# Kernel optimization log

Measured on AMD Instinct MI355X. Metric: run time of the kernel, lower is better.

Reference implementation:

```python
import jax, jax.numpy as jnp
import numpy as np

B, D, E, H, O, TOPK = 16384, 256, 8, 128, 1, 2
THRESHOLD = 0.5
NUM_SCALES = 3
TAUS = np.linspace(5.0, 20.0, NUM_SCALES)  # MSLIFNeuron tau_range=(5,20), num_scales=3


def setup_inputs() -> dict:
    key = jax.random.key(0)
    ks = jax.random.split(key, 10)
    s = lambda fan: 1.0 / np.sqrt(fan)
    return {
        "features": jax.random.normal(ks[0], (B, D), jnp.float32),
        "Wg": jax.random.normal(ks[1], (D, E), jnp.float32) * s(D),
        "W1": jax.random.normal(ks[2], (E, D, H), jnp.float32) * s(D),
        "b1": jnp.zeros((E, H), jnp.float32),
        "Wp": jax.random.normal(ks[3], (E, H, H), jnp.float32) * s(H),
        "bp": jnp.zeros((E, H), jnp.float32),
        "mix_logit": jnp.zeros((E,), jnp.float32),
        "Wo": jax.random.normal(ks[4], (E, H, O), jnp.float32) * s(H),
        "bo": jnp.zeros((E, O), jnp.float32),
    }


def _mslif_spikes(x):
    # multi-scale LIF, single step from zero state: v_s = x * (1 - exp(-dt/tau_s))
    decays = jnp.asarray(1.0 - np.exp(-1.0 / TAUS), x.dtype)  # [S]
    v = x[:, None, :] * decays[None, :, None]                  # [B,S,D]
    return (v > THRESHOLD).astype(x.dtype).mean(axis=1)        # [B,D]


def reference(features, Wg, W1, b1, Wp, bp, mix_logit, Wo, bo):
    # gating: softmax over experts, top-k renormalized
    gate = jax.nn.softmax(features @ Wg, axis=-1)              # [B,E]
    _, idx = jax.lax.top_k(gate, TOPK)                         # [B,K]
    mask = jax.nn.one_hot(idx, E, dtype=gate.dtype).sum(1)     # [B,E]
    w = gate * mask
    w = w / (w.sum(-1, keepdims=True) + 1e-10)

    # spike generator (computed in expert forward; not used downstream)
    _spikes = _mslif_spikes(features)

    # NeuroDynArch expert: static core + plasticity mix
    core = jax.nn.relu(jnp.einsum('bd,edh->beh', features, W1) + b1[None])
    plast = jnp.tanh(jnp.einsum('beh,ehk->bek', core, Wp) + bp[None])
    mix = jax.nn.sigmoid(mix_logit)[None, :, None]             # [1,E,1]
    mixed = core * (1.0 - mix) + plast * mix                   # [B,E,H]
    out_e = jnp.einsum('beh,eho->beo', mixed, Wo) + bo[None]   # [B,E,O]
    return jnp.einsum('beo,be->bo', out_e, w)                  # [B,O]
```

## Files before the change

kernel.cpp:

```cpp
#include <hip/hip_runtime.h>

#define BB 16384
#define DD 256
#define EE 8
#define HH 128

typedef __attribute__((ext_vector_type(8))) short short8;
typedef __attribute__((ext_vector_type(4))) float f32x4;

__device__ __forceinline__ ushort f2bf(float f){
    const unsigned u = __float_as_uint(f);
    return (ushort)((u + 0x7fffu + ((u >> 16) & 1u)) >> 16);
}
__device__ __forceinline__ float bf2f(ushort s){
    return __uint_as_float(((unsigned)s) << 16);
}
__device__ __forceinline__ float fast_tanh(float v){
    v = fminf(fmaxf(v, -15.0f), 15.0f);
    const float a = __expf(2.0f * v);
    return (a - 1.0f) / (a + 1.0f);
}
__device__ __forceinline__ void gload_lds16(const void* g, void* l){
    __builtin_amdgcn_global_load_lds(
        (const __attribute__((address_space(1))) unsigned*)g,
        (__attribute__((address_space(3))) unsigned*)l, 16, 0, 0);
}

__global__ __launch_bounds__(256) void transpose_kernel(
    const float* __restrict__ W1, const float* __restrict__ Wp,
    ushort* __restrict__ W1t, ushort* __restrict__ Wpt, int* __restrict__ counts)
{
    __shared__ float tile[64 * 68];
    int b = blockIdx.x;
    const int t = threadIdx.x;
    if (b == 0 && t < EE) counts[t] = 0;
    const float* src; ushort* dst; int K;
    int k0, h0;
    if (b < 64){
        const int e = b >> 3, kt = (b >> 1) & 3, ht = b & 1;
        src = W1 + (size_t)e * DD * HH;  dst = W1t + (size_t)e * HH * DD;
        K = DD; k0 = kt * 64; h0 = ht * 64;
    } else {
        b -= 64;
        const int e = b >> 2, kt = (b >> 1) & 1, ht = b & 1;
        src = Wp + (size_t)e * HH * HH;  dst = Wpt + (size_t)e * HH * HH;
        K = HH; k0 = kt * 64; h0 = ht * 64;
    }
    #pragma unroll
    for (int j = 0; j < 4; j++){
        const int idx = t + 256 * j;
        const int kk = idx >> 4, hh = (idx & 15) * 4;
        const float4 v = *(const float4*)(src + (size_t)(k0 + kk) * HH + h0 + hh);
        *(float4*)&tile[kk * 68 + hh] = v;
    }
    __syncthreads();
    #pragma unroll
    for (int j = 0; j < 4; j++){
        const int idx = t + 256 * j;
        const int hh = idx >> 4, kk = (idx & 15) * 4;
        ushort4 o;
        o.x = f2bf(tile[(kk + 0) * 68 + hh]);
        o.y = f2bf(tile[(kk + 1) * 68 + hh]);
        o.z = f2bf(tile[(kk + 2) * 68 + hh]);
        o.w = f2bf(tile[(kk + 3) * 68 + hh]);
        *(ushort4*)&dst[(size_t)(h0 + hh) * K + k0 + kk] = o;
    }
}

__global__ __launch_bounds__(256) void routing_kernel(
    const float* __restrict__ x, const float* __restrict__ Wg,
    int* __restrict__ counts, int* __restrict__ rowids, float* __restrict__ wgts,
    float* __restrict__ out, ushort* __restrict__ xbf)
{
    __shared__ __align__(16) float WgT[EE][DD];
    __shared__ int   le[64];
    __shared__ float lw[64];
    __shared__ int   loff[64];
    __shared__ int   lcount[EE];
    __shared__ int   lbase[EE];

    const int t = threadIdx.x;
    const int rowBase = blockIdx.x * 32;
    if (t < 32) out[rowBase + t] = 0.0f;
    {
        const float4* g = (const float4*)(Wg + t * EE);
        const float4 a = g[0], b = g[1];
        WgT[0][t] = a.x; WgT[1][t] = a.y; WgT[2][t] = a.z; WgT[3][t] = a.w;
        WgT[4][t] = b.x; WgT[5][t] = b.y; WgT[6][t] = b.z; WgT[7][t] = b.w;
    }
    if (t < EE) lcount[t] = 0;
    __syncthreads();

    const int lane = t & 63;
    const int wid  = t >> 6;

    for (int it = 0; it < 8; it++){
        const int slot = wid * 8 + it;
        const int row  = rowBase + slot;
        const float4 xv = *(const float4*)(x + row * DD + lane * 4);
        {
            ushort4 o;
            o.x = f2bf(xv.x); o.y = f2bf(xv.y); o.z = f2bf(xv.z); o.w = f2bf(xv.w);
            *(ushort4*)&xbf[(size_t)row * DD + lane * 4] = o;
        }
        float p[EE];
        #pragma unroll
        for (int e = 0; e < EE; e++){
            const float4 w = *(const float4*)&WgT[e][lane * 4];
            p[e] = xv.x * w.x + xv.y * w.y + xv.z * w.z + xv.w * w.w;
        }
        #pragma unroll
        for (int off = 32; off >= 1; off >>= 1){
            #pragma unroll
            for (int e = 0; e < EE; e++) p[e] += __shfl_down(p[e], off, 64);
        }
        if (lane == 0){
            int e0 = 0; float l0 = p[0];
            #pragma unroll
            for (int e = 1; e < EE; e++){ if (p[e] > l0){ l0 = p[e]; e0 = e; } }
            int e1 = -1; float l1 = -3.0e38f;
            #pragma unroll
            for (int e = 0; e < EE; e++){ if (e != e0 && p[e] > l1){ l1 = p[e]; e1 = e; } }
            const float tt  = __expf(l1 - l0);
            const float inv = 1.0f / (1.0f + tt);
            le[slot]      = e0;  lw[slot]      = inv;
            le[32 + slot] = e1;  lw[32 + slot] = tt * inv;
        }
    }
    __syncthreads();
    if (t < 64) loff[t] = atomicAdd(&lcount[le[t]], 1);
    __syncthreads();
    if (t < EE) lbase[t] = atomicAdd(&counts[t], lcount[t]);
    __syncthreads();
    if (t < 64){
        const int e   = le[t];
        const int pos = lbase[e] + loff[t];
        rowids[e * BB + pos] = rowBase + (t & 31);
        wgts[e * BB + pos]   = lw[t];
    }
}

#define CS_S 136

__global__ __launch_bounds__(256, 2) void expert_kernel(
    const ushort* __restrict__ xbf,
    const ushort* __restrict__ W1t, const float* __restrict__ b1,
    const ushort* __restrict__ Wpt, const float* __restrict__ bp,
    const float* __restrict__ mix_logit,
    const float* __restrict__ Wo, const float* __restrict__ bo,
    const int* __restrict__ counts, const int* __restrict__ rowids,
    const float* __restrict__ wgts, float* __restrict__ out)
{
    const int me    = blockIdx.y;
    const int cnt   = counts[me];
    const int start = blockIdx.x * 64;
    if (start >= cnt) return;

    __shared__ ushort Xs[64 * DD];
    __shared__ ushort coreS[64 * CS_S];
    __shared__ int   rid_s[64];
    __shared__ float w_s[64];

    const int t = threadIdx.x;
    if (t < 64){
        const int idx = start + t;
        if (idx < cnt){ rid_s[t] = rowids[me * BB + idx]; w_s[t] = wgts[me * BB + idx]; }
        else          { rid_s[t] = 0;                     w_s[t] = 0.0f; }
    }
    __syncthreads();

    const int lane = t & 63;
    const int w    = t >> 6;

    {
        const int rsub = lane >> 5;
        const int c    = lane & 31;
        #pragma unroll
        for (int i = 0; i < 8; i++){
            const int row = w * 16 + i * 2 + rsub;
            const int sc  = c ^ (row & 7);
            const ushort* gp = xbf + (size_t)rid_s[row] * DD + sc * 8;
            gload_lds16(gp, &Xs[(w * 16 + i * 2) * DD]);
        }
    }
    asm volatile("s_waitcnt vmcnt(0)" ::: "memory");
    __syncthreads();

    const int m16  = lane & 15;
    const int q    = lane >> 4;
    const int r0   = 32 * (w >> 1);
    const int c0   = 64 * (w & 1);
    const int swz  = m16 & 7;

    f32x4 acc[2][4];
    #pragma unroll
    for (int ct = 0; ct < 4; ct++){
        const float bj = b1[me * HH + c0 + ct * 16 + m16];
        #pragma unroll
        for (int rt = 0; rt < 2; rt++) acc[rt][ct] = (f32x4){bj, bj, bj, bj};
    }
    const ushort* W1te = W1t + (size_t)me * HH * DD;
    #pragma unroll
    for (int ks = 0; ks < 8; ks++){
        const int kc = ks * 4 + q;
        short8 af[2], bf[4];
        #pragma unroll
        for (int rt = 0; rt < 2; rt++)
            af[rt] = *(const short8*)&Xs[(r0 + rt * 16 + m16) * DD + ((kc ^ swz) * 8)];
        #pragma unroll
        for (int ct = 0; ct < 4; ct++)
            bf[ct] = *(const short8*)&W1te[(size_t)(c0 + ct * 16 + m16) * DD + ks * 32 + q * 8];
        #pragma unroll
        for (int rt = 0; rt < 2; rt++)
            #pragma unroll
            for (int ct = 0; ct < 4; ct++)
                acc[rt][ct] = __builtin_amdgcn_mfma_f32_16x16x32_bf16(af[rt], bf[ct], acc[rt][ct], 0, 0, 0);
    }

    #pragma unroll
    for (int rt = 0; rt < 2; rt++)
        #pragma unroll
        for (int ct = 0; ct < 4; ct++)
            #pragma unroll
            for (int j = 0; j < 4; j++){
                const int row = r0 + rt * 16 + q * 4 + j;
                const int col = c0 + ct * 16 + m16;
                coreS[row * CS_S + col] = f2bf(fmaxf(acc[rt][ct][j], 0.0f));
            }
    __syncthreads();

    #pragma unroll
    for (int ct = 0; ct < 4; ct++){
        const float bj = bp[me * HH + c0 + ct * 16 + m16];
        #pragma unroll
        for (int rt = 0; rt < 2; rt++) acc[rt][ct] = (f32x4){bj, bj, bj, bj};
    }
    const ushort* Wpte = Wpt + (size_t)me * HH * HH;
    #pragma unroll
    for (int ks = 0; ks < 4; ks++){
        const int k0 = ks * 32;
        short8 af[2], bf[4];
        #pragma unroll
        for (int rt = 0; rt < 2; rt++)
            af[rt] = *(const short8*)&coreS[(r0 + rt * 16 + m16) * CS_S + k0 + q * 8];
        #pragma unroll
        for (int ct = 0; ct < 4; ct++)
            bf[ct] = *(const short8*)&Wpte[(size_t)(c0 + ct * 16 + m16) * HH + k0 + q * 8];
        #pragma unroll
        for (int rt = 0; rt < 2; rt++)
            #pragma unroll
            for (int ct = 0; ct < 4; ct++)
                acc[rt][ct] = __builtin_amdgcn_mfma_f32_16x16x32_bf16(af[rt], bf[ct], acc[rt][ct], 0, 0, 0);
    }

    const float mv  = 1.0f / (1.0f + __expf(-mix_logit[me]));
    const float om  = 1.0f - mv;
    const float bov = bo[me];
    float wo[4];
    #pragma unroll
    for (int ct = 0; ct < 4; ct++) wo[ct] = Wo[me * HH + c0 + ct * 16 + m16];

    float red[2][4];
    #pragma unroll
    for (int rt = 0; rt < 2; rt++)
        #pragma unroll
        for (int j = 0; j < 4; j++){
            float s = 0.0f;
            const int row = r0 + rt * 16 + q * 4 + j;
            #pragma unroll
            for (int ct = 0; ct < 4; ct++){
                const int col = c0 + ct * 16 + m16;
                const float pl = fast_tanh(acc[rt][ct][j]);
                const float cv = bf2f(coreS[row * CS_S + col]);
                s = fmaf(om * cv + mv * pl, wo[ct], s);
            }
            red[rt][j] = s;
        }
    #pragma unroll
    for (int off = 8; off >= 1; off >>= 1)
        #pragma unroll
        for (int rt = 0; rt < 2; rt++)
            #pragma unroll
            for (int j = 0; j < 4; j++)
                red[rt][j] += __shfl_xor(red[rt][j], off, 64);

    if (m16 == 0){
        const float bb = (c0 == 0) ? bov : 0.0f;
        #pragma unroll
        for (int rt = 0; rt < 2; rt++)
            #pragma unroll
            for (int j = 0; j < 4; j++){
                const int row = r0 + rt * 16 + q * 4 + j;
                const float ww = w_s[row];
                if (ww != 0.0f) atomicAdd(&out[rid_s[row]], (red[rt][j] + bb) * ww);
            }
    }
}

extern "C" void kernel_launch(void* const* d_in, const int* in_sizes, int n_in,
                              void* d_out, int out_size, void* d_ws, size_t ws_size,
                              hipStream_t stream) {
    (void)in_sizes; (void)n_in; (void)out_size; (void)ws_size;
    const float* x   = (const float*)d_in[0];
    const float* Wg  = (const float*)d_in[1];
    const float* W1  = (const float*)d_in[2];
    const float* b1  = (const float*)d_in[3];
    const float* Wp  = (const float*)d_in[4];
    const float* bp  = (const float*)d_in[5];
    const float* ml  = (const float*)d_in[6];
    const float* Wo  = (const float*)d_in[7];
    const float* bo  = (const float*)d_in[8];
    float* out = (float*)d_out;

    char* ws = (char*)d_ws;
    int*    counts = (int*)ws;
    int*    rowids = (int*)(ws + 256);
    float*  wgts   = (float*)(ws + 256 + (size_t)EE * BB * 4);
    ushort* W1t    = (ushort*)(ws + 256 + 2 * (size_t)EE * BB * 4);
    ushort* Wpt    = W1t + (size_t)EE * HH * DD;
    ushort* xbf    = Wpt + (size_t)EE * HH * HH;

    transpose_kernel<<<96, 256, 0, stream>>>(W1, Wp, W1t, Wpt, counts);
    routing_kernel<<<BB / 32, 256, 0, stream>>>(x, Wg, counts, rowids, wgts, out, xbf);
    expert_kernel<<<dim3(BB / 64, EE), 256, 0, stream>>>(
        xbf, W1t, b1, Wpt, bp, ml, Wo, bo, counts, rowids, wgts, out);
}
```

Measured before the change: 120.2 us.

## Fuse transpose, routing and expert kernels into one cooperative persistent launch

Merges the three kernels into a single cooperative-groups kernel of 512 persistent blocks. Grid-wide syncs replace the kernel boundaries, and the expert phase loops over (expert, chunk) work items. The per-expert counters are padded onto separate cache lines to reduce atomic contention. The aim is to cut launch overhead and inter-kernel gaps, at the cost of grid-sync latency and occupancy limits, with a fallback to the three-kernel path if a cooperative launch is not possible.

```diff
diff --git a/kernel.cpp b/kernel.cpp
--- a/kernel.cpp
+++ b/kernel.cpp
@@ -1,9 +1,15 @@
 #include <hip/hip_runtime.h>
+#include <hip/hip_cooperative_groups.h>
+
+namespace cg = cooperative_groups;
 
 #define BB 16384
 #define DD 256
 #define EE 8
 #define HH 128
+#define NBLK 512
+#define CPAD 32
+#define CS_S 136
 
 typedef __attribute__((ext_vector_type(8))) short short8;
 typedef __attribute__((ext_vector_type(4))) float f32x4;
@@ -26,14 +32,23 @@
         (__attribute__((address_space(3))) unsigned*)l, 16, 0, 0);
 }
 
-__global__ __launch_bounds__(256) void transpose_kernel(
+struct RT {
+    float WgT[EE][DD];
+    int   le[64];
+    float lw[64];
+    int   loff[64];
+    int   lcount[EE];
+    int   lbase[EE];
+};
+struct P1 { float tile[64 * 68]; RT rt; };
+struct P3 { ushort Xs[64 * DD]; ushort coreS[64 * CS_S];
+            int rid[64]; float wgt[64]; };
+union ShU { P1 p1; P3 p3; };
+
+__device__ __forceinline__ void transpose_body(int b, int t,
     const float* __restrict__ W1, const float* __restrict__ Wp,
-    ushort* __restrict__ W1t, ushort* __restrict__ Wpt, int* __restrict__ counts)
-{
-    __shared__ float tile[64 * 68];
-    int b = blockIdx.x;
-    const int t = threadIdx.x;
-    if (b == 0 && t < EE) counts[t] = 0;
+    ushort* __restrict__ W1t, ushort* __restrict__ Wpt, float* tile)
+{
     const float* src; ushort* dst; int K;
     int k0, h0;
     if (b < 64){
@@ -67,28 +82,19 @@
     }
 }
 
-__global__ __launch_bounds__(256) void routing_kernel(
+__device__ __forceinline__ void routing_p1(int bid, int t,
     const float* __restrict__ x, const float* __restrict__ Wg,
-    int* __restrict__ counts, int* __restrict__ rowids, float* __restrict__ wgts,
-    float* __restrict__ out, ushort* __restrict__ xbf)
-{
-    __shared__ __align__(16) float WgT[EE][DD];
-    __shared__ int   le[64];
-    __shared__ float lw[64];
-    __shared__ int   loff[64];
-    __shared__ int   lcount[EE];
-    __shared__ int   lbase[EE];
-
-    const int t = threadIdx.x;
-    const int rowBase = blockIdx.x * 32;
+    float* __restrict__ out, ushort* __restrict__ xbf, RT* rt)
+{
+    const int rowBase = bid * 32;
     if (t < 32) out[rowBase + t] = 0.0f;
     {
         const float4* g = (const float4*)(Wg + t * EE);
         const float4 a = g[0], b = g[1];
-        WgT[0][t] = a.x; WgT[1][t] = a.y; WgT[2][t] = a.z; WgT[3][t] = a.w;
-        WgT[4][t] = b.x; WgT[5][t] = b.y; WgT[6][t] = b.z; WgT[7][t] = b.w;
-    }
-    if (t < EE) lcount[t] = 0;
+        rt->WgT[0][t] = a.x; rt->WgT[1][t] = a.y; rt->WgT[2][t] = a.z; rt->WgT[3][t] = a.w;
+        rt->WgT[4][t] = b.x; rt->WgT[5][t] = b.y; rt->WgT[6][t] = b.z; rt->WgT[7][t] = b.w;
+    }
+    if (t < EE) rt->lcount[t] = 0;
     __syncthreads();
 
     const int lane = t & 63;
@@ -106,7 +112,7 @@
         float p[EE];
         #pragma unroll
         for (int e = 0; e < EE; e++){
-            const float4 w = *(const float4*)&WgT[e][lane * 4];
+            const float4 w = *(const float4*)&rt->WgT[e][lane * 4];
             p[e] = xv.x * w.x + xv.y * w.y + xv.z * w.z + xv.w * w.w;
         }
         #pragma unroll
@@ -123,49 +129,42 @@
             for (int e = 0; e < EE; e++){ if (e != e0 && p[e] > l1){ l1 = p[e]; e1 = e; } }
             const float tt  = __expf(l1 - l0);
             const float inv = 1.0f / (1.0f + tt);
-            le[slot]      = e0;  lw[slot]      = inv;
-            le[32 + slot] = e1;  lw[32 + slot] = tt * inv;
-        }
-    }
-    __syncthreads();
-    if (t < 64) loff[t] = atomicAdd(&lcount[le[t]], 1);
-    __syncthreads();
-    if (t < EE) lbase[t] = atomicAdd(&counts[t], lcount[t]);
+            rt->le[slot]      = e0;  rt->lw[slot]      = inv;
+            rt->le[32 + slot] = e1;  rt->lw[32 + slot] = tt * inv;
+        }
+    }
+}
+
+__device__ __forceinline__ void routing_p2(int bid, int t,
+    int* counts, int* __restrict__ rowids, float* __restrict__ wgts, RT* rt)
+{
+    __syncthreads();
+    if (t < 64) rt->loff[t] = atomicAdd(&rt->lcount[rt->le[t]], 1);
+    __syncthreads();
+    if (t < EE) rt->lbase[t] = atomicAdd(&counts[t * CPAD], rt->lcount[t]);
     __syncthreads();
     if (t < 64){
-        const int e   = le[t];
-        const int pos = lbase[e] + loff[t];
-        rowids[e * BB + pos] = rowBase + (t & 31);
-        wgts[e * BB + pos]   = lw[t];
-    }
-}
-
-#define CS_S 136
-
-__global__ __launch_bounds__(256, 2) void expert_kernel(
+        const int e   = rt->le[t];
+        const int pos = rt->lbase[e] + rt->loff[t];
+        rowids[e * BB + pos] = bid * 32 + (t & 31);
+        wgts[e * BB + pos]   = rt->lw[t];
+    }
+}
+
+__device__ void expert_chunk(int me, int start, int cnt, int t,
     const ushort* __restrict__ xbf,
     const ushort* __restrict__ W1t, const float* __restrict__ b1,
     const ushort* __restrict__ Wpt, const float* __restrict__ bp,
     const float* __restrict__ mix_logit,
     const float* __restrict__ Wo, const float* __restrict__ bo,
-    const int* __restrict__ counts, const int* __restrict__ rowids,
-    const float* __restrict__ wgts, float* __restrict__ out)
-{
-    const int me    = blockIdx.y;
-    const int cnt   = counts[me];
-    const int start = blockIdx.x * 64;
-    if (start >= cnt) return;
-
-    __shared__ ushort Xs[64 * DD];
-    __shared__ ushort coreS[64 * CS_S];
-    __shared__ int   rid_s[64];
-    __shared__ float w_s[64];
-
-    const int t = threadIdx.x;
+    const int* __restrict__ rowids, const float* __restrict__ wgts,
+    float* __restrict__ out, P3* p3)
+{
+    __syncthreads();
     if (t < 64){
         const int idx = start + t;
-        if (idx < cnt){ rid_s[t] = rowids[me * BB + idx]; w_s[t] = wgts[me * BB + idx]; }
-        else          { rid_s[t] = 0;                     w_s[t] = 0.0f; }
+        if (idx < cnt){ p3->rid[t] = rowids[me * BB + idx]; p3->wgt[t] = wgts[me * BB + idx]; }
+        else          { p3->rid[t] = 0;                     p3->wgt[t] = 0.0f; }
     }
     __syncthreads();
 
@@ -179,8 +178,8 @@
         for (int i = 0; i < 8; i++){
             const int row = w * 16 + i * 2 + rsub;
             const int sc  = c ^ (row & 7);
-            const ushort* gp = xbf + (size_t)rid_s[row] * DD + sc * 8;
-            gload_lds16(gp, &Xs[(w * 16 + i * 2) * DD]);
+            const ushort* gp = xbf + (size_t)p3->rid[row] * DD + sc * 8;
+            gload_lds16(gp, &p3->Xs[(w * 16 + i * 2) * DD]);
         }
     }
     asm volatile("s_waitcnt vmcnt(0)" ::: "memory");
@@ -203,18 +202,18 @@
     #pragma unroll
     for (int ks = 0; ks < 8; ks++){
         const int kc = ks * 4 + q;
-        short8 af[2], bf[4];
-        #pragma unroll
-        for (int rt = 0; rt < 2; rt++)
-            af[rt] = *(const short8*)&Xs[(r0 + rt * 16 + m16) * DD + ((kc ^ swz) * 8)];
+        short8 af[2], bfr[4];
+        #pragma unroll
+        for (int rt = 0; rt < 2; rt++)
+            af[rt] = *(const short8*)&p3->Xs[(r0 + rt * 16 + m16) * DD + ((kc ^ swz) * 8)];
         #pragma unroll
         for (int ct = 0; ct < 4; ct++)
-            bf[ct] = *(const short8*)&W1te[(size_t)(c0 + ct * 16 + m16) * DD + ks * 32 + q * 8];
+            bfr[ct] = *(const short8*)&W1te[(size_t)(c0 + ct * 16 + m16) * DD + ks * 32 + q * 8];
         #pragma unroll
         for (int rt = 0; rt < 2; rt++)
             #pragma unroll
             for (int ct = 0; ct < 4; ct++)
-                acc[rt][ct] = __builtin_amdgcn_mfma_f32_16x16x32_bf16(af[rt], bf[ct], acc[rt][ct], 0, 0, 0);
+                acc[rt][ct] = __builtin_amdgcn_mfma_f32_16x16x32_bf16(af[rt], bfr[ct], acc[rt][ct], 0, 0, 0);
     }
 
     #pragma unroll
@@ -225,7 +224,7 @@
             for (int j = 0; j < 4; j++){
                 const int row = r0 + rt * 16 + q * 4 + j;
                 const int col = c0 + ct * 16 + m16;
-                coreS[row * CS_S + col] = f2bf(fmaxf(acc[rt][ct][j], 0.0f));
+                p3->coreS[row * CS_S + col] = f2bf(fmaxf(acc[rt][ct][j], 0.0f));
             }
     __syncthreads();
 
@@ -239,18 +238,18 @@
     #pragma unroll
     for (int ks = 0; ks < 4; ks++){
         const int k0 = ks * 32;
-        short8 af[2], bf[4];
-        #pragma unroll
-        for (int rt = 0; rt < 2; rt++)
-            af[rt] = *(const short8*)&coreS[(r0 + rt * 16 + m16) * CS_S + k0 + q * 8];
+        short8 af[2], bfr[4];
+        #pragma unroll
+        for (int rt = 0; rt < 2; rt++)
+            af[rt] = *(const short8*)&p3->coreS[(r0 + rt * 16 + m16) * CS_S + k0 + q * 8];
         #pragma unroll
         for (int ct = 0; ct < 4; ct++)
-            bf[ct] = *(const short8*)&Wpte[(size_t)(c0 + ct * 16 + m16) * HH + k0 + q * 8];
+            bfr[ct] = *(const short8*)&Wpte[(size_t)(c0 + ct * 16 + m16) * HH + k0 + q * 8];
         #pragma unroll
         for (int rt = 0; rt < 2; rt++)
             #pragma unroll
             for (int ct = 0; ct < 4; ct++)
-                acc[rt][ct] = __builtin_amdgcn_mfma_f32_16x16x32_bf16(af[rt], bf[ct], acc[rt][ct], 0, 0, 0);
+                acc[rt][ct] = __builtin_amdgcn_mfma_f32_16x16x32_bf16(af[rt], bfr[ct], acc[rt][ct], 0, 0, 0);
     }
 
     const float mv  = 1.0f / (1.0f + __expf(-mix_logit[me]));
@@ -271,7 +270,7 @@
             for (int ct = 0; ct < 4; ct++){
                 const int col = c0 + ct * 16 + m16;
                 const float pl = fast_tanh(acc[rt][ct][j]);
-                const float cv = bf2f(coreS[row * CS_S + col]);
+                const float cv = bf2f(p3->coreS[row * CS_S + col]);
                 s = fmaf(om * cv + mv * pl, wo[ct], s);
             }
             red[rt][j] = s;
@@ -291,10 +290,82 @@
             #pragma unroll
             for (int j = 0; j < 4; j++){
                 const int row = r0 + rt * 16 + q * 4 + j;
-                const float ww = w_s[row];
-                if (ww != 0.0f) atomicAdd(&out[rid_s[row]], (red[rt][j] + bb) * ww);
+                const float ww = p3->wgt[row];
+                if (ww != 0.0f) atomicAdd(&out[p3->rid[row]], (red[rt][j] + bb) * ww);
             }
     }
+}
+
+__global__ __launch_bounds__(256, 2) void fused_kernel(
+    const float* __restrict__ x, const float* __restrict__ Wg,
+    const float* __restrict__ W1, const float* __restrict__ b1,
+    const float* __restrict__ Wp, const float* __restrict__ bp,
+    const float* __restrict__ ml, const float* __restrict__ Wo,
+    const float* __restrict__ bo,
+    int* counts, int* rowids, float* wgts,
+    ushort* W1t, ushort* Wpt, ushort* xbf, float* out)
+{
+    __shared__ ShU sh;
+    const int bid = blockIdx.x;
+    const int t   = threadIdx.x;
+
+    if (bid == 0 && t < EE) counts[t * CPAD] = 0;
+    if (bid < 96) transpose_body(bid, t, W1, Wp, W1t, Wpt, sh.p1.tile);
+    routing_p1(bid, t, x, Wg, out, xbf, &sh.p1.rt);
+
+    cg::this_grid().sync();
+
+    routing_p2(bid, t, counts, rowids, wgts, &sh.p1.rt);
+
+    cg::this_grid().sync();
+
+    #pragma unroll 1
+    for (int v = bid; v < EE * 256; v += NBLK){
+        const int me    = v & 7;
+        const int start = (v >> 3) * 64;
+        const int cnt   = counts[me * CPAD];
+        if (start < cnt)
+            expert_chunk(me, start, cnt, t, xbf, W1t, b1, Wpt, bp, ml, Wo, bo,
+                         rowids, wgts, out, &sh.p3);
+    }
+}
+
+__global__ __launch_bounds__(256) void transpose_kernel(
+    const float* __restrict__ W1, const float* __restrict__ Wp,
+    ushort* __restrict__ W1t, ushort* __restrict__ Wpt, int* __restrict__ counts)
+{
+    __shared__ float tile[64 * 68];
+    const int t = threadIdx.x;
+    if (blockIdx.x == 0 && t < EE) counts[t * CPAD] = 0;
+    transpose_body(blockIdx.x, t, W1, Wp, W1t, Wpt, tile);
+}
+
+__global__ __launch_bounds__(256) void routing_kernel(
+    const float* __restrict__ x, const float* __restrict__ Wg,
+    int* counts, int* __restrict__ rowids, float* __restrict__ wgts,
+    float* __restrict__ out, ushort* __restrict__ xbf)
+{
+    __shared__ RT rt;
+    routing_p1(blockIdx.x, threadIdx.x, x, Wg, out, xbf, &rt);
+    routing_p2(blockIdx.x, threadIdx.x, counts, rowids, wgts, &rt);
+}
+
+__global__ __launch_bounds__(256, 2) void expert_kernel(
+    const ushort* __restrict__ xbf,
+    const ushort* __restrict__ W1t, const float* __restrict__ b1,
+    const ushort* __restrict__ Wpt, const float* __restrict__ bp,
+    const float* __restrict__ ml,
+    const float* __restrict__ Wo, const float* __restrict__ bo,
+    const int* __restrict__ counts, const int* __restrict__ rowids,
+    const float* __restrict__ wgts, float* __restrict__ out)
+{
+    const int me    = blockIdx.y;
+    const int cnt   = counts[me * CPAD];
+    const int start = blockIdx.x * 64;
+    if (start >= cnt) return;
+    __shared__ P3 p3;
+    expert_chunk(me, start, cnt, threadIdx.x, xbf, W1t, b1, Wpt, bp, ml, Wo, bo,
+                 rowids, wgts, out, &p3);
 }
 
 extern "C" void kernel_launch(void* const* d_in, const int* in_sizes, int n_in,
@@ -314,11 +385,31 @@
 
     char* ws = (char*)d_ws;
     int*    counts = (int*)ws;
-    int*    rowids = (int*)(ws + 256);
-    float*  wgts   = (float*)(ws + 256 + (size_t)EE * BB * 4);
-    ushort* W1t    = (ushort*)(ws + 256 + 2 * (size_t)EE * BB * 4);
+    int*    rowids = (int*)(ws + 1024);
+    float*  wgts   = (float*)(ws + 1024 + (size_t)EE * BB * 4);
+    ushort* W1t    = (ushort*)(ws + 1024 + 2 * (size_t)EE * BB * 4);
     ushort* Wpt    = W1t + (size_t)EE * HH * DD;
     ushort* xbf    = Wpt + (size_t)EE * HH * HH;
+
+    static int coop_ok = -1;
+    if (coop_ok < 0){
+        int dev = 0; hipGetDevice(&dev);
+        int sup = 0; hipDeviceGetAttribute(&sup, hipDeviceAttributeCooperativeLaunch, dev);
+        int ncu = 0; hipDeviceGetAttribute(&ncu, hipDeviceAttributeMultiprocessorCount, dev);
+        int nb  = 0; hipOccupancyMaxActiveBlocksPerMultiprocessor(&nb, fused_kernel, 256, 0);
+        coop_ok = (sup && ncu > 0 && nb * ncu >= NBLK) ? 1 : 0;
+    }
+
+    if (coop_ok == 1){
+        void* args[] = { (void*)&x, (void*)&Wg, (void*)&W1, (void*)&b1, (void*)&Wp,
+                         (void*)&bp, (void*)&ml, (void*)&Wo, (void*)&bo,
+                         (void*)&counts, (void*)&rowids, (void*)&wgts,
+                         (void*)&W1t, (void*)&Wpt, (void*)&xbf, (void*)&out };
+        hipError_t err = hipLaunchCooperativeKernel(fused_kernel, dim3(NBLK), dim3(256),
+                                                    args, 0, stream);
+        if (err == hipSuccess) return;
+        coop_ok = 0;
+    }
 
     transpose_kernel<<<96, 256, 0, stream>>>(W1, Wp, W1t, Wpt, counts);
     routing_kernel<<<BB / 32, 256, 0, stream>>>(x, Wg, counts, rowids, wgts, out, xbf);
```

New measurement: 139.7 us. 1.16x slower.

## Merge transpose and routing into one prep kernel with segmented histogram dispatch

Applied to the files above, without the earlier changes.

Merges the weight-transpose and routing kernels into a single launch, with blocks split by index. The global atomic counters are replaced by a per-block histogram plus fixed segments, and each expert block does a prefix scan and binary search to find its rows. The expert kernel drops the LDS staging of X and reads bf16 rows straight from global memory, which frees LDS so the occupancy hint can go from 2 to 3. This removes one launch, the global atomics and the counter zeroing, at the cost of a redundant scan in every expert block and uncoalesced global A-fragment loads.

```diff
diff --git a/kernel.cpp b/kernel.cpp
--- a/kernel.cpp
+++ b/kernel.cpp
@@ -4,6 +4,9 @@
 #define DD 256
 #define EE 8
 #define HH 128
+#define RBLK 512
+#define TBLK 96
+#define CS_S 136
 
 typedef __attribute__((ext_vector_type(8))) short short8;
 typedef __attribute__((ext_vector_type(4))) float f32x4;
@@ -20,20 +23,20 @@
     const float a = __expf(2.0f * v);
     return (a - 1.0f) / (a + 1.0f);
 }
-__device__ __forceinline__ void gload_lds16(const void* g, void* l){
-    __builtin_amdgcn_global_load_lds(
-        (const __attribute__((address_space(1))) unsigned*)g,
-        (__attribute__((address_space(3))) unsigned*)l, 16, 0, 0);
-}
-
-__global__ __launch_bounds__(256) void transpose_kernel(
+
+struct RT {
+    float WgT[EE][DD];
+    int   le[64];
+    float lw[64];
+    int   loff[64];
+    int   lcount[EE];
+};
+union ShU { float tile[64 * 68]; RT rt; };
+
+__device__ __forceinline__ void transpose_body(int b, int t,
     const float* __restrict__ W1, const float* __restrict__ Wp,
-    ushort* __restrict__ W1t, ushort* __restrict__ Wpt, int* __restrict__ counts)
+    ushort* __restrict__ W1t, ushort* __restrict__ Wpt, float* tile)
 {
-    __shared__ float tile[64 * 68];
-    int b = blockIdx.x;
-    const int t = threadIdx.x;
-    if (b == 0 && t < EE) counts[t] = 0;
     const float* src; ushort* dst; int K;
     int k0, h0;
     if (b < 64){
@@ -67,28 +70,30 @@
     }
 }
 
-__global__ __launch_bounds__(256) void routing_kernel(
+__global__ __launch_bounds__(256) void prep_kernel(
     const float* __restrict__ x, const float* __restrict__ Wg,
-    int* __restrict__ counts, int* __restrict__ rowids, float* __restrict__ wgts,
-    float* __restrict__ out, ushort* __restrict__ xbf)
+    const float* __restrict__ W1, const float* __restrict__ Wp,
+    ushort* __restrict__ W1t, ushort* __restrict__ Wpt,
+    ushort* __restrict__ xbf, float* __restrict__ out,
+    int* __restrict__ hist, int* __restrict__ seg_rid, float* __restrict__ seg_wgt)
 {
-    __shared__ __align__(16) float WgT[EE][DD];
-    __shared__ int   le[64];
-    __shared__ float lw[64];
-    __shared__ int   loff[64];
-    __shared__ int   lcount[EE];
-    __shared__ int   lbase[EE];
-
+    __shared__ ShU sh;
     const int t = threadIdx.x;
-    const int rowBase = blockIdx.x * 32;
+    if (blockIdx.x < TBLK){
+        transpose_body(blockIdx.x, t, W1, Wp, W1t, Wpt, sh.tile);
+        return;
+    }
+    RT* rt = &sh.rt;
+    const int rb = blockIdx.x - TBLK;
+    const int rowBase = rb * 32;
     if (t < 32) out[rowBase + t] = 0.0f;
     {
         const float4* g = (const float4*)(Wg + t * EE);
         const float4 a = g[0], b = g[1];
-        WgT[0][t] = a.x; WgT[1][t] = a.y; WgT[2][t] = a.z; WgT[3][t] = a.w;
-        WgT[4][t] = b.x; WgT[5][t] = b.y; WgT[6][t] = b.z; WgT[7][t] = b.w;
-    }
-    if (t < EE) lcount[t] = 0;
+        rt->WgT[0][t] = a.x; rt->WgT[1][t] = a.y; rt->WgT[2][t] = a.z; rt->WgT[3][t] = a.w;
+        rt->WgT[4][t] = b.x; rt->WgT[5][t] = b.y; rt->WgT[6][t] = b.z; rt->WgT[7][t] = b.w;
+    }
+    if (t < EE) rt->lcount[t] = 0;
     __syncthreads();
 
     const int lane = t & 63;
@@ -106,8 +111,8 @@
         float p[EE];
         #pragma unroll
         for (int e = 0; e < EE; e++){
-            const float4 w = *(const float4*)&WgT[e][lane * 4];
-            p[e] = xv.x * w.x + xv.y * w.y + xv.z * w.z + xv.w * w.w;
+            const float4 ww = *(const float4*)&rt->WgT[e][lane * 4];
+            p[e] = xv.x * ww.x + xv.y * ww.y + xv.z * ww.z + xv.w * ww.w;
         }
         #pragma unroll
         for (int off = 32; off >= 1; off >>= 1){
@@ -123,74 +128,84 @@
             for (int e = 0; e < EE; e++){ if (e != e0 && p[e] > l1){ l1 = p[e]; e1 = e; } }
             const float tt  = __expf(l1 - l0);
             const float inv = 1.0f / (1.0f + tt);
-            le[slot]      = e0;  lw[slot]      = inv;
-            le[32 + slot] = e1;  lw[32 + slot] = tt * inv;
-        }
-    }
-    __syncthreads();
-    if (t < 64) loff[t] = atomicAdd(&lcount[le[t]], 1);
-    __syncthreads();
-    if (t < EE) lbase[t] = atomicAdd(&counts[t], lcount[t]);
-    __syncthreads();
+            rt->le[slot]      = e0;  rt->lw[slot]      = inv;
+            rt->le[32 + slot] = e1;  rt->lw[32 + slot] = tt * inv;
+        }
+    }
+    __syncthreads();
+    if (t < 64) rt->loff[t] = atomicAdd(&rt->lcount[rt->le[t]], 1);
+    __syncthreads();
+    if (t < EE) hist[t * RBLK + rb] = rt->lcount[t];
     if (t < 64){
-        const int e   = le[t];
-        const int pos = lbase[e] + loff[t];
-        rowids[e * BB + pos] = rowBase + (t & 31);
-        wgts[e * BB + pos]   = lw[t];
-    }
-}
-
-#define CS_S 136
-
-__global__ __launch_bounds__(256, 2) void expert_kernel(
+        const int e = rt->le[t];
+        const int o = (e * RBLK + rb) * 32 + rt->loff[t];
+        seg_rid[o] = rowBase + (t & 31);
+        seg_wgt[o] = rt->lw[t];
+    }
+}
+
+__global__ __launch_bounds__(256, 3) void expert_kernel(
     const ushort* __restrict__ xbf,
     const ushort* __restrict__ W1t, const float* __restrict__ b1,
     const ushort* __restrict__ Wpt, const float* __restrict__ bp,
     const float* __restrict__ mix_logit,
     const float* __restrict__ Wo, const float* __restrict__ bo,
-    const int* __restrict__ counts, const int* __restrict__ rowids,
-    const float* __restrict__ wgts, float* __restrict__ out)
+    const int* __restrict__ hist, const int* __restrict__ seg_rid,
+    const float* __restrict__ seg_wgt, float* __restrict__ out)
 {
-    const int me    = blockIdx.y;
-    const int cnt   = counts[me];
+    __shared__ ushort coreS[64 * CS_S];
+    __shared__ int    Ps[RBLK + 1];
+    __shared__ int    rid_s[64];
+    __shared__ float  w_s[64];
+
+    const int me = blockIdx.y;
+    const int t  = threadIdx.x;
+
+    if (t < 64){
+        int h[8], incl[8];
+        int s = 0;
+        #pragma unroll
+        for (int i = 0; i < 8; i++){ h[i] = hist[me * RBLK + t * 8 + i]; s += h[i]; incl[i] = s; }
+        int run = s;
+        #pragma unroll
+        for (int off = 1; off < 64; off <<= 1){
+            const int n = __shfl_up(run, off, 64);
+            if (t >= off) run += n;
+        }
+        const int excl = run - s;
+        #pragma unroll
+        for (int i = 0; i < 8; i++) Ps[t * 8 + i] = excl + incl[i] - h[i];
+        if (t == 63) Ps[RBLK] = excl + s;
+    }
+    __syncthreads();
+    const int cnt   = Ps[RBLK];
     const int start = blockIdx.x * 64;
     if (start >= cnt) return;
 
-    __shared__ ushort Xs[64 * DD];
-    __shared__ ushort coreS[64 * CS_S];
-    __shared__ int   rid_s[64];
-    __shared__ float w_s[64];
-
-    const int t = threadIdx.x;
     if (t < 64){
-        const int idx = start + t;
-        if (idx < cnt){ rid_s[t] = rowids[me * BB + idx]; w_s[t] = wgts[me * BB + idx]; }
-        else          { rid_s[t] = 0;                     w_s[t] = 0.0f; }
+        const int s = start + t;
+        if (s < cnt){
+            int lo = 0, hi = RBLK - 1;
+            while (lo < hi){
+                const int mid = (lo + hi + 1) >> 1;
+                if (Ps[mid] <= s) lo = mid; else hi = mid - 1;
+            }
+            const int o = (me * RBLK + lo) * 32 + (s - Ps[lo]);
+            rid_s[t] = seg_rid[o];
+            w_s[t]   = seg_wgt[o];
+        } else { rid_s[t] = 0; w_s[t] = 0.0f; }
     }
     __syncthreads();
 
     const int lane = t & 63;
     const int w    = t >> 6;
-
-    {
-        const int rsub = lane >> 5;
-        const int c    = lane & 31;
-        #pragma unroll
-        for (int i = 0; i < 8; i++){
-            const int row = w * 16 + i * 2 + rsub;
-            const int sc  = c ^ (row & 7);
-            const ushort* gp = xbf + (size_t)rid_s[row] * DD + sc * 8;
-            gload_lds16(gp, &Xs[(w * 16 + i * 2) * DD]);
-        }
-    }
-    asm volatile("s_waitcnt vmcnt(0)" ::: "memory");
-    __syncthreads();
-
     const int m16  = lane & 15;
     const int q    = lane >> 4;
     const int r0   = 32 * (w >> 1);
     const int c0   = 64 * (w & 1);
-    const int swz  = m16 & 7;
+
+    const ushort* xrA = xbf + (size_t)rid_s[r0 + m16]      * DD;
+    const ushort* xrB = xbf + (size_t)rid_s[r0 + 16 + m16] * DD;
 
     f32x4 acc[2][4];
     #pragma unroll
@@ -202,19 +217,17 @@
     const ushort* W1te = W1t + (size_t)me * HH * DD;
     #pragma unroll
     for (int ks = 0; ks < 8; ks++){
-        const int kc = ks * 4 + q;
-        short8 af[2], bf[4];
-        #pragma unroll
-        for (int rt = 0; rt < 2; rt++)
-            af[rt] = *(const short8*)&Xs[(r0 + rt * 16 + m16) * DD + ((kc ^ swz) * 8)];
+        short8 af[2], bfr[4];
+        af[0] = *(const short8*)&xrA[ks * 32 + q * 8];
+        af[1] = *(const short8*)&xrB[ks * 32 + q * 8];
         #pragma unroll
         for (int ct = 0; ct < 4; ct++)
-            bf[ct] = *(const short8*)&W1te[(size_t)(c0 + ct * 16 + m16) * DD + ks * 32 + q * 8];
+            bfr[ct] = *(const short8*)&W1te[(size_t)(c0 + ct * 16 + m16) * DD + ks * 32 + q * 8];
         #pragma unroll
         for (int rt = 0; rt < 2; rt++)
             #pragma unroll
             for (int ct = 0; ct < 4; ct++)
-                acc[rt][ct] = __builtin_amdgcn_mfma_f32_16x16x32_bf16(af[rt], bf[ct], acc[rt][ct], 0, 0, 0);
+                acc[rt][ct] = __builtin_amdgcn_mfma_f32_16x16x32_bf16(af[rt], bfr[ct], acc[rt][ct], 0, 0, 0);
     }
 
     #pragma unroll
@@ -239,18 +252,18 @@
     #pragma unroll
     for (int ks = 0; ks < 4; ks++){
         const int k0 = ks * 32;
-        short8 af[2], bf[4];
+        short8 af[2], bfr[4];
         #pragma unroll
         for (int rt = 0; rt < 2; rt++)
             af[rt] = *(const short8*)&coreS[(r0 + rt * 16 + m16) * CS_S + k0 + q * 8];
         #pragma unroll
         for (int ct = 0; ct < 4; ct++)
-            bf[ct] = *(const short8*)&Wpte[(size_t)(c0 + ct * 16 + m16) * HH + k0 + q * 8];
+            bfr[ct] = *(const short8*)&Wpte[(size_t)(c0 + ct * 16 + m16) * HH + k0 + q * 8];
         #pragma unroll
         for (int rt = 0; rt < 2; rt++)
             #pragma unroll
             for (int ct = 0; ct < 4; ct++)
-                acc[rt][ct] = __builtin_amdgcn_mfma_f32_16x16x32_bf16(af[rt], bf[ct], acc[rt][ct], 0, 0, 0);
+                acc[rt][ct] = __builtin_amdgcn_mfma_f32_16x16x32_bf16(af[rt], bfr[ct], acc[rt][ct], 0, 0, 0);
     }
 
     const float mv  = 1.0f / (1.0f + __expf(-mix_logit[me]));
@@ -313,15 +326,15 @@
     float* out = (float*)d_out;
 
     char* ws = (char*)d_ws;
-    int*    counts = (int*)ws;
-    int*    rowids = (int*)(ws + 256);
-    float*  wgts   = (float*)(ws + 256 + (size_t)EE * BB * 4);
-    ushort* W1t    = (ushort*)(ws + 256 + 2 * (size_t)EE * BB * 4);
-    ushort* Wpt    = W1t + (size_t)EE * HH * DD;
-    ushort* xbf    = Wpt + (size_t)EE * HH * HH;
-
-    transpose_kernel<<<96, 256, 0, stream>>>(W1, Wp, W1t, Wpt, counts);
-    routing_kernel<<<BB / 32, 256, 0, stream>>>(x, Wg, counts, rowids, wgts, out, xbf);
+    int*    hist    = (int*)ws;
+    int*    seg_rid = (int*)(ws + (16 << 10));
+    float*  seg_wgt = (float*)(ws + (16 << 10) + (512 << 10));
+    ushort* W1t     = (ushort*)(ws + (16 << 10) + 2 * (512 << 10));
+    ushort* Wpt     = W1t + (size_t)EE * HH * DD;
+    ushort* xbf     = Wpt + (size_t)EE * HH * HH;
+
+    prep_kernel<<<TBLK + RBLK, 256, 0, stream>>>(
+        x, Wg, W1, Wp, W1t, Wpt, xbf, out, hist, seg_rid, seg_wgt);
     expert_kernel<<<dim3(BB / 64, EE), 256, 0, stream>>>(
-        xbf, W1t, b1, Wpt, bp, ml, Wo, bo, counts, rowids, wgts, out);
-}
+        xbf, W1t, b1, Wpt, bp, ml, Wo, bo, hist, seg_rid, seg_wgt, out);
+}
```

Result: slower. 147.0 us (+22.3%).
